# Optimization experiments

Measured on AMD Instinct MI355X. Metric: run time of the kernel, lower is better.

The kernel has to match this reference:

```python
import jax, jax.numpy as jnp
import numpy as np

B, T, C = 4, 2048, 1024
H, D = 16, 64  # num_heads, head_size


def setup_inputs() -> dict:
    key = jax.random.key(0)
    ks = jax.random.split(key, 5)
    s = 0.02
    x = jax.random.normal(ks[0], (B, T, C), dtype=jnp.float32)
    Wq = jax.random.normal(ks[1], (H, C, D), dtype=jnp.float32) * s
    Wk = jax.random.normal(ks[2], (H, C, D), dtype=jnp.float32) * s
    Wv = jax.random.normal(ks[3], (H, C, D), dtype=jnp.float32) * s
    Wp = jax.random.normal(ks[4], (C, H * D), dtype=jnp.float32) * s  # Linear(H*D, C) weight
    bp = jnp.zeros((C,), dtype=jnp.float32)
    return {"x": x, "Wq": Wq, "Wk": Wk, "Wv": Wv, "Wp": Wp, "bp": bp}


def reference(x, Wq, Wk, Wv, Wp, bp):
    # per-head projections (all heads batched): [B,T,C] x [H,C,D] -> [B,H,T,D]
    q = jnp.einsum('btc,hcd->bhtd', x, Wq)
    k = jnp.einsum('btc,hcd->bhtd', x, Wk)
    v = jnp.einsum('btc,hcd->bhtd', x, Wv)
    scale = 1.0 / jnp.sqrt(jnp.asarray(D, dtype=x.dtype))
    scores = jnp.einsum('bhtd,bhsd->bhts', q, k) * scale  # [B,H,T,T]
    causal = jnp.tril(jnp.ones((T, T), dtype=bool))
    scores = jnp.where(causal, scores, -jnp.inf)
    w = jax.nn.softmax(scores, axis=-1)
    out = jnp.einsum('bhts,bhsd->bhtd', w, v)  # [B,H,T,D]
    out = out.transpose(0, 2, 1, 3).reshape(B, T, H * D)  # concat heads
    return out @ Wp.T + bp  # projection (dropout is identity in eval)
```

## Files before the change

### kernel.cpp

```cpp
#include <hip/hip_runtime.h>
#include <stdint.h>


typedef unsigned short u16;
typedef __attribute__((ext_vector_type(8))) short    s16x8;
typedef __attribute__((ext_vector_type(4))) float    f32x4;
typedef __attribute__((ext_vector_type(2))) uint32_t u32x2;


__device__ __forceinline__ u16 f2b(float f) {
  union { float f; uint32_t u; } v; v.f = f;
  uint32_t r = v.u + 0x7FFFu + ((v.u >> 16) & 1u);
  return (u16)(r >> 16);
}

__device__ __forceinline__ uint32_t cvtpk(float a, float b) {
  uint32_t r;
  asm("v_cvt_pk_bf16_f32 %0, %1, %2" : "=v"(r) : "v"(a), "v"(b));
  return r;
}

__device__ __forceinline__ float vexp2(float x) {
  float r;
  asm("v_exp_f32 %0, %1" : "=v"(r) : "v"(x));
  return r;
}

__device__ __forceinline__ f32x4 mfma_bf16(s16x8 a, s16x8 b, f32x4 c) {
  asm("v_mfma_f32_16x16x32_bf16 %0, %1, %2, %0" : "+v"(c) : "v"(a), "v"(b));
  return c;
}

__device__ __forceinline__ void gload_lds16(const void* g, void* l) {
  __builtin_amdgcn_global_load_lds(
      (__attribute__((address_space(1))) void*)(uintptr_t)g,
      (__attribute__((address_space(3))) void*)(uint32_t)(uintptr_t)l,
      16, 0, 0);
}


__global__ void cvt_all_kernel(const float* __restrict__ x, const float* __restrict__ Wq,
                               const float* __restrict__ Wk, const float* __restrict__ Wv,
                               const float* __restrict__ Wp, u16* __restrict__ xb,
                               u16* __restrict__ wqkvb, u16* __restrict__ wpb) {
  int bid = blockIdx.x;
  if (bid < 4608) {
    const float* src = (bid < 4096) ? x : Wp;
    u16* dst = (bid < 4096) ? xb : wpb;
    size_t i = (size_t)((bid < 4096) ? bid : (bid - 4096)) * 256 + threadIdx.x;
    const f32x4* pp = (const f32x4*)(src + i * 8);
    f32x4 a = pp[0], b2 = pp[1];
    s16x8 o;
    o[0]=(short)f2b(a[0]); o[1]=(short)f2b(a[1]); o[2]=(short)f2b(a[2]); o[3]=(short)f2b(a[3]);
    o[4]=(short)f2b(b2[0]); o[5]=(short)f2b(b2[1]); o[6]=(short)f2b(b2[2]); o[7]=(short)f2b(b2[3]);
    *(s16x8*)(dst + i * 8) = o;
  } else {
    int idx = (bid - 4608) * 256 + threadIdx.x;
    int sel = idx >> 20;
    int rem = idx & 1048575;
    int n = rem >> 10, c = rem & 1023;
    int h = n >> 6, d = n & 63;
    const float* W = (sel == 0) ? Wq : ((sel == 1) ? Wk : Wv);
    wqkvb[idx] = f2b(W[h * 65536 + c * 64 + d]);
  }
}


template <int MODE>
__global__ __launch_bounds__(256) void gemm_bt_kernel(
    const u16* __restrict__ A, const u16* __restrict__ B, void* __restrict__ Cout,
    const float* __restrict__ bias, u16* __restrict__ vTout, int K, int ldc)
{
  __shared__ __attribute__((aligned(16))) u16 As[128 * 64];
  __shared__ __attribute__((aligned(16))) u16 Bs[128 * 64];

  const int tid  = threadIdx.x;
  const int lane = tid & 63;
  const int w    = tid >> 6;
  const int wm   = w >> 1, wn = w & 1;
  const int g    = lane >> 4;
  const int li   = lane & 15;
  const size_t bm = (size_t)blockIdx.x * 128;
  const size_t bn = (size_t)blockIdx.y * 128;

  f32x4 acc[4][4] = {};

  const int kIters = K >> 6;
  for (int kt = 0; kt < kIters; ++kt) {
    const int kb = kt * 64;
#pragma unroll
    for (int i = 0; i < 4; ++i) {
      int c = i * 256 + tid;
      int row = c >> 3, sl = c & 7;
      int ss = sl ^ (row & 7);
      gload_lds16(A + (bm + row) * K + kb + ss * 8, &As[c * 8]);
      gload_lds16(B + (bn + row) * K + kb + ss * 8, &Bs[c * 8]);
    }
    __syncthreads();
#pragma unroll
    for (int ks = 0; ks < 2; ++ks) {
      s16x8 af[4], bfr[4];
#pragma unroll
      for (int f = 0; f < 4; ++f) {
        int ra = wm * 64 + f * 16 + li;
        int sa = (ks * 4 + g) ^ (ra & 7);
        af[f] = *(const s16x8*)&As[ra * 64 + sa * 8];
        int rb = wn * 64 + f * 16 + li;
        int sb = (ks * 4 + g) ^ (rb & 7);
        bfr[f] = *(const s16x8*)&Bs[rb * 64 + sb * 8];
      }
#pragma unroll
      for (int mi = 0; mi < 4; ++mi)
#pragma unroll
        for (int ni = 0; ni < 4; ++ni)
          acc[mi][ni] = mfma_bf16(af[mi], bfr[ni], acc[mi][ni]);
    }
    __syncthreads();
  }

  if constexpr (MODE == 1) {
#pragma unroll
    for (int ni = 0; ni < 4; ++ni) {
      size_t col = bn + wn * 64 + ni * 16 + li;
      float bv = bias[col];
#pragma unroll
      for (int mi = 0; mi < 4; ++mi)
#pragma unroll
        for (int r = 0; r < 4; ++r) {
          size_t row = bm + wm * 64 + mi * 16 + g * 4 + r;
          ((float*)Cout)[row * ldc + col] = acc[mi][ni][r] + bv;
        }
    }
  } else {
    if (bn < 2048) {
#pragma unroll
      for (int ni = 0; ni < 4; ++ni) {
        size_t col = bn + wn * 64 + ni * 16 + li;
#pragma unroll
        for (int mi = 0; mi < 4; ++mi)
#pragma unroll
          for (int r = 0; r < 4; ++r) {
            size_t row = bm + wm * 64 + mi * 16 + g * 4 + r;
            ((u16*)Cout)[row * ldc + col] = f2b(acc[mi][ni][r]);
          }
      }
    } else {
      const int hb = (int)((bn - 2048) >> 6) + wn;
      const int bb = (int)(bm >> 11);
      const int t0b = ((int)bm & 2047) + wm * 64 + g * 4;
      u16* vrow = vTout + (size_t)((bb * 16 + hb) * 64) * 2048;
#pragma unroll
      for (int ni = 0; ni < 4; ++ni) {
        u16* vd_ = vrow + (size_t)(ni * 16 + li) * 2048;
#pragma unroll
        for (int mi = 0; mi < 4; ++mi) {
          u32x2 wv = { cvtpk(acc[mi][ni][0], acc[mi][ni][1]),
                       cvtpk(acc[mi][ni][2], acc[mi][ni][3]) };
          *(u32x2*)&vd_[t0b + mi * 16] = wv;
        }
      }
    }
  }
}


__global__ __launch_bounds__(256, 4) void attn_kernel(const u16* __restrict__ qkv,
                                                      const u16* __restrict__ vT,
                                                      u16* __restrict__ out) {
  __shared__ __attribute__((aligned(16))) u16 Ks[2][64 * 64];
  __shared__ __attribute__((aligned(16))) u16 Vs[2][64 * 64];
  __shared__ __attribute__((aligned(16))) u16 Ps[4][16 * 64];

  const int id  = blockIdx.x;
  const int xcd = id & 7;
  const int rr  = id >> 3;
  const int bh  = xcd * 8 + (rr & 7);
  const int p   = rr >> 3;

  const int b = bh >> 4, h = bh & 15;
  const int tid = threadIdx.x;
  const int lane = tid & 63;
  const int w = tid >> 6;
  const int g = lane >> 4, li = lane & 15;

  const int tA = 31 - p;
  const int nA = tA + 1;
  const int nTot = 33;

  const u16* kbase = qkv + (size_t)(b * 2048) * 3072 + 1024 + h * 64;
  const u16* vtb   = vT + (size_t)bh * 64 * 2048;
  u16* pl = Ps[w];

  const int srow = tid >> 3;
  const int ssl0 = (tid & 7) ^ (srow & 7);
  const int kge0 = srow * 3072 + ssl0 * 8;
  const int vge0 = srow * 2048 + ssl0 * 8;
  u16* const kd0 = &Ks[0][tid * 8];
  u16* const vd0 = &Vs[0][tid * 8];

  int foff[2][4];
#pragma unroll
  for (int kk = 0; kk < 2; ++kk)
#pragma unroll
    for (int fj = 0; fj < 4; ++fj) {
      int rk = fj * 16 + li;
      foff[kk][fj] = rk * 64 + (((kk * 4 + g) ^ (rk & 7)) * 8);
    }
  const int lsw = li & 14;
  int pwoff[4], proff[2];
#pragma unroll
  for (int fj = 0; fj < 4; ++fj) pwoff[fj] = li * 64 + (((4 * fj + g) ^ lsw) * 4);
#pragma unroll
  for (int kk = 0; kk < 2; ++kk) proff[kk] = li * 64 + (((8 * kk + 2 * g) ^ lsw) * 4);

  auto stage = [&](int buf, int j0) {
    const u16* kp = kbase + (size_t)j0 * 3072;
    const u16* vp = vtb + j0;
    u16* kd = kd0 + buf * 4096;
    u16* vd = vd0 + buf * 4096;
    gload_lds16(kp + kge0, kd);
    gload_lds16(kp + kge0 + 32 * 3072, kd + 2048);
    gload_lds16(vp + vge0, vd);
    gload_lds16(vp + vge0 + 32 * 2048, vd + 2048);
  };

  stage(0, 0);
  __syncthreads();

  s16x8 qf[2];
  f32x4 oacc[4];
  float mrow = -1e30f, lrowp = 0.f;
  int qglob = 0;
  const float cexp = 0.18033688011112042f;
  const float thr = 8.0f;

  for (int s = 0; s < nTot; ++s) {
    const int cur = s & 1;
    const bool inA = s < nA;
    const int t  = inA ? s : s - nA;
    const int qt = inA ? tA : p;
    const int j0 = t * 64;

    if (s + 1 < nTot) {
      int t1 = (s + 1 < nA) ? (s + 1) : (s + 1 - nA);
      stage(cur ^ 1, t1 * 64);
    }

    if (t == 0) {
      qglob = qt * 64 + w * 16 + li;
      const u16* qbase = qkv + (size_t)(b * 2048 + qglob) * 3072 + h * 64;
#pragma unroll
      for (int kk = 0; kk < 2; ++kk)
        qf[kk] = *(const s16x8*)&qbase[kk * 32 + g * 8];
      mrow = -1e30f; lrowp = 0.f;
#pragma unroll
      for (int fd = 0; fd < 4; ++fd) oacc[fd] = (f32x4)0.f;
    }

    const u16* ksb = &Ks[0][0] + cur * 4096;
    const u16* vsb = &Vs[0][0] + cur * 4096;

    f32x4 sfr[4] = {};
    __builtin_amdgcn_s_setprio(1);
#pragma unroll
    for (int kk = 0; kk < 2; ++kk) {
      s16x8 kf[4];
#pragma unroll
      for (int fj = 0; fj < 4; ++fj) kf[fj] = *(const s16x8*)&ksb[foff[kk][fj]];
#pragma unroll
      for (int fj = 0; fj < 4; ++fj) sfr[fj] = mfma_bf16(kf[fj], qf[kk], sfr[fj]);
    }
    __builtin_amdgcn_s_setprio(0);

    if (t == qt) {
#pragma unroll
      for (int fj = 0; fj < 4; ++fj)
#pragma unroll
        for (int r = 0; r < 4; ++r) {
          int jj = j0 + fj * 16 + g * 4 + r;
          if (jj > qglob) sfr[fj][r] = -1e30f;
        }
    }

    float mx = sfr[0][0];
#pragma unroll
    for (int fj = 0; fj < 4; ++fj)
#pragma unroll
      for (int r = 0; r < 4; ++r) mx = fmaxf(mx, sfr[fj][r]);

    bool need = (mx - mrow) * cexp > thr;
    if (__any(need)) {
      float m0 = mx;
      m0 = fmaxf(m0, __shfl_xor(m0, 16));
      m0 = fmaxf(m0, __shfl_xor(m0, 32));
      float mnew = fmaxf(mrow, m0);
      float sc = vexp2((mrow - mnew) * cexp);
      mrow = mnew;
      lrowp *= sc;
#pragma unroll
      for (int fd = 0; fd < 4; ++fd)
#pragma unroll
        for (int r = 0; r < 4; ++r) oacc[fd][r] *= sc;
    }

    float rs = 0.f;
#pragma unroll
    for (int fj = 0; fj < 4; ++fj) {
      float p0 = vexp2((sfr[fj][0] - mrow) * cexp);
      float p1 = vexp2((sfr[fj][1] - mrow) * cexp);
      float p2 = vexp2((sfr[fj][2] - mrow) * cexp);
      float p3 = vexp2((sfr[fj][3] - mrow) * cexp);
      rs += (p0 + p1) + (p2 + p3);
      u32x2 wv = { cvtpk(p0, p1), cvtpk(p2, p3) };
      *(u32x2*)&pl[pwoff[fj]] = wv;
    }
    lrowp += rs;

    __builtin_amdgcn_s_setprio(1);
#pragma unroll
    for (int kk = 0; kk < 2; ++kk) {
      s16x8 pf = *(const s16x8*)&pl[proff[kk]];
      s16x8 vf[4];
#pragma unroll
      for (int fd = 0; fd < 4; ++fd) vf[fd] = *(const s16x8*)&vsb[foff[kk][fd]];
#pragma unroll
      for (int fd = 0; fd < 4; ++fd) oacc[fd] = mfma_bf16(vf[fd], pf, oacc[fd]);
    }
    __builtin_amdgcn_s_setprio(0);

    if (t == qt) {
      float lr = lrowp;
      lr += __shfl_xor(lr, 16);
      lr += __shfl_xor(lr, 32);
      float inv = 1.f / lr;
      u16* ob = out + (size_t)(b * 2048 + qglob) * 1024 + h * 64;
#pragma unroll
      for (int fd = 0; fd < 4; ++fd) {
        u32x2 wv = { cvtpk(oacc[fd][0] * inv, oacc[fd][1] * inv),
                     cvtpk(oacc[fd][2] * inv, oacc[fd][3] * inv) };
        *(u32x2*)&ob[fd * 16 + g * 4] = wv;
      }
    }

    __syncthreads();
  }
}


extern "C" void kernel_launch(void* const* d_in, const int* in_sizes, int n_in,
                              void* d_out, int out_size, void* d_ws, size_t ws_size,
                              hipStream_t stream) {
  const float* x  = (const float*)d_in[0];
  const float* Wq = (const float*)d_in[1];
  const float* Wk = (const float*)d_in[2];
  const float* Wv = (const float*)d_in[3];
  const float* Wp = (const float*)d_in[4];
  const float* bp = (const float*)d_in[5];
  (void)in_sizes; (void)n_in; (void)out_size; (void)ws_size;

  char* ws = (char*)d_ws;
  u16* xb    = (u16*)(ws);
  u16* wqkvb = (u16*)(ws + 16777216);
  u16* wpb   = (u16*)(ws + 23068672);
  u16* qkv   = (u16*)(ws + 25165824);
  u16* vT    = (u16*)(ws + 75497472);
  u16* ao    = (u16*)(ws + 92274688);

  cvt_all_kernel<<<16896, 256, 0, stream>>>(x, Wq, Wk, Wv, Wp, xb, wqkvb, wpb);

  gemm_bt_kernel<2><<<dim3(64, 24), 256, 0, stream>>>(
      xb, wqkvb, (void*)qkv, nullptr, vT, 1024, 3072);

  attn_kernel<<<1024, 256, 0, stream>>>(qkv, vT, ao);

  gemm_bt_kernel<1><<<dim3(64, 8), 256, 0, stream>>>(
      ao, wpb, d_out, bp, nullptr, 1024, 1024);
}
```

Before: 154.8 us.

## Split KV tile across warp pairs with 32-row Q per warp and merge partial softmax

```diff
diff --git a/kernel.cpp b/kernel.cpp
--- a/kernel.cpp
+++ b/kernel.cpp
@@ -169,7 +169,7 @@
                                                       u16* __restrict__ out) {
   __shared__ __attribute__((aligned(16))) u16 Ks[2][64 * 64];
   __shared__ __attribute__((aligned(16))) u16 Vs[2][64 * 64];
-  __shared__ __attribute__((aligned(16))) u16 Ps[4][16 * 64];
+  __shared__ __attribute__((aligned(16))) u16 Ps[4][32 * 32];
 
   const int id  = blockIdx.x;
   const int xcd = id & 7;
@@ -182,6 +182,8 @@
   const int lane = tid & 63;
   const int w = tid >> 6;
   const int g = lane >> 4, li = lane & 15;
+  const int wq  = w & 1;
+  const int kvh = w >> 1;
 
   const int tA = 31 - p;
   const int nA = tA + 1;
@@ -198,20 +200,29 @@
   u16* const kd0 = &Ks[0][tid * 8];
   u16* const vd0 = &Vs[0][tid * 8];
 
-  int foff[2][4];
+  int foffK[2][2];
 #pragma unroll
   for (int kk = 0; kk < 2; ++kk)
 #pragma unroll
-    for (int fj = 0; fj < 4; ++fj) {
-      int rk = fj * 16 + li;
-      foff[kk][fj] = rk * 64 + (((kk * 4 + g) ^ (rk & 7)) * 8);
-    }
-  const int lsw = li & 14;
-  int pwoff[4], proff[2];
-#pragma unroll
-  for (int fj = 0; fj < 4; ++fj) pwoff[fj] = li * 64 + (((4 * fj + g) ^ lsw) * 4);
-#pragma unroll
-  for (int kk = 0; kk < 2; ++kk) proff[kk] = li * 64 + (((8 * kk + 2 * g) ^ lsw) * 4);
+    for (int fj = 0; fj < 2; ++fj) {
+      int rk = kvh * 32 + fj * 16 + li;
+      foffK[kk][fj] = rk * 64 + (((kk * 4 + g) ^ (rk & 7)) * 8);
+    }
+  int foffV[4];
+#pragma unroll
+  for (int fd = 0; fd < 4; ++fd) {
+    int rv = fd * 16 + li;
+    foffV[fd] = rv * 64 + (((kvh * 4 + g) ^ (rv & 7)) * 8);
+  }
+  const int psw = li & 3;
+  int pwoff[2][2], proff[2];
+#pragma unroll
+  for (int fm = 0; fm < 2; ++fm) {
+#pragma unroll
+    for (int fj = 0; fj < 2; ++fj)
+      pwoff[fm][fj] = (fm * 16 + li) * 32 + (((fj * 2 + (g >> 1)) ^ psw) * 8) + (g & 1) * 4;
+    proff[fm] = (fm * 16 + li) * 32 + ((g ^ psw) * 8);
+  }
 
   auto stage = [&](int buf, int j0) {
     const u16* kp = kbase + (size_t)j0 * 3072;
@@ -227,10 +238,10 @@
   stage(0, 0);
   __syncthreads();
 
-  s16x8 qf[2];
-  f32x4 oacc[4];
-  float mrow = -1e30f, lrowp = 0.f;
-  int qglob = 0;
+  s16x8 qf[2][2];
+  f32x4 oacc[2][4];
+  float mrow[2], lrowp[2];
+  int qg0 = 0;
   const float cexp = 0.18033688011112042f;
   const float thr = 8.0f;
 
@@ -247,98 +258,160 @@
     }
 
     if (t == 0) {
-      qglob = qt * 64 + w * 16 + li;
-      const u16* qbase = qkv + (size_t)(b * 2048 + qglob) * 3072 + h * 64;
-#pragma unroll
-      for (int kk = 0; kk < 2; ++kk)
-        qf[kk] = *(const s16x8*)&qbase[kk * 32 + g * 8];
-      mrow = -1e30f; lrowp = 0.f;
-#pragma unroll
-      for (int fd = 0; fd < 4; ++fd) oacc[fd] = (f32x4)0.f;
+      qg0 = qt * 64 + wq * 32 + li;
+#pragma unroll
+      for (int fm = 0; fm < 2; ++fm) {
+        const u16* qbase = qkv + (size_t)(b * 2048 + qg0 + fm * 16) * 3072 + h * 64;
+#pragma unroll
+        for (int kk = 0; kk < 2; ++kk)
+          qf[fm][kk] = *(const s16x8*)&qbase[kk * 32 + g * 8];
+        mrow[fm] = -1e30f; lrowp[fm] = 0.f;
+#pragma unroll
+        for (int fd = 0; fd < 4; ++fd) oacc[fm][fd] = (f32x4)0.f;
+      }
     }
 
     const u16* ksb = &Ks[0][0] + cur * 4096;
     const u16* vsb = &Vs[0][0] + cur * 4096;
 
-    f32x4 sfr[4] = {};
-    __builtin_amdgcn_s_setprio(1);
-#pragma unroll
-    for (int kk = 0; kk < 2; ++kk) {
-      s16x8 kf[4];
-#pragma unroll
-      for (int fj = 0; fj < 4; ++fj) kf[fj] = *(const s16x8*)&ksb[foff[kk][fj]];
-#pragma unroll
-      for (int fj = 0; fj < 4; ++fj) sfr[fj] = mfma_bf16(kf[fj], qf[kk], sfr[fj]);
-    }
-    __builtin_amdgcn_s_setprio(0);
+    const bool skipw = (t == qt) && (kvh == 1) && (wq == 0);
+    if (!skipw) {
+      f32x4 sfr[2][2] = {};
+      __builtin_amdgcn_s_setprio(1);
+#pragma unroll
+      for (int kk = 0; kk < 2; ++kk) {
+        s16x8 kf[2];
+#pragma unroll
+        for (int fj = 0; fj < 2; ++fj) kf[fj] = *(const s16x8*)&ksb[foffK[kk][fj]];
+#pragma unroll
+        for (int fm = 0; fm < 2; ++fm)
+#pragma unroll
+          for (int fj = 0; fj < 2; ++fj)
+            sfr[fm][fj] = mfma_bf16(kf[fj], qf[fm][kk], sfr[fm][fj]);
+      }
+      __builtin_amdgcn_s_setprio(0);
+
+      if (t == qt) {
+#pragma unroll
+        for (int fm = 0; fm < 2; ++fm)
+#pragma unroll
+          for (int fj = 0; fj < 2; ++fj)
+#pragma unroll
+            for (int r = 0; r < 4; ++r) {
+              int jj = j0 + kvh * 32 + fj * 16 + g * 4 + r;
+              if (jj > qg0 + fm * 16) sfr[fm][fj][r] = -1e30f;
+            }
+      }
+
+      float mx[2];
+#pragma unroll
+      for (int fm = 0; fm < 2; ++fm) {
+        float m0 = sfr[fm][0][0];
+#pragma unroll
+        for (int fj = 0; fj < 2; ++fj)
+#pragma unroll
+          for (int r = 0; r < 4; ++r) m0 = fmaxf(m0, sfr[fm][fj][r]);
+        mx[fm] = m0;
+      }
+      bool need = ((mx[0] - mrow[0]) * cexp > thr) | ((mx[1] - mrow[1]) * cexp > thr);
+      if (__any(need)) {
+#pragma unroll
+        for (int fm = 0; fm < 2; ++fm) {
+          float m0 = mx[fm];
+          m0 = fmaxf(m0, __shfl_xor(m0, 16));
+          m0 = fmaxf(m0, __shfl_xor(m0, 32));
+          float mnew = fmaxf(mrow[fm], m0);
+          float sc = vexp2((mrow[fm] - mnew) * cexp);
+          mrow[fm] = mnew;
+          lrowp[fm] *= sc;
+#pragma unroll
+          for (int fd = 0; fd < 4; ++fd)
+#pragma unroll
+            for (int r = 0; r < 4; ++r) oacc[fm][fd][r] *= sc;
+        }
+      }
+
+#pragma unroll
+      for (int fm = 0; fm < 2; ++fm) {
+        float rs = 0.f;
+#pragma unroll
+        for (int fj = 0; fj < 2; ++fj) {
+          float p0 = vexp2((sfr[fm][fj][0] - mrow[fm]) * cexp);
+          float p1 = vexp2((sfr[fm][fj][1] - mrow[fm]) * cexp);
+          float p2 = vexp2((sfr[fm][fj][2] - mrow[fm]) * cexp);
+          float p3 = vexp2((sfr[fm][fj][3] - mrow[fm]) * cexp);
+          rs += (p0 + p1) + (p2 + p3);
+          u32x2 wv = { cvtpk(p0, p1), cvtpk(p2, p3) };
+          *(u32x2*)&pl[pwoff[fm][fj]] = wv;
+        }
+        lrowp[fm] += rs;
+      }
+
+      __builtin_amdgcn_s_setprio(1);
+      s16x8 vf[4];
+#pragma unroll
+      for (int fd = 0; fd < 4; ++fd) vf[fd] = *(const s16x8*)&vsb[foffV[fd]];
+#pragma unroll
+      for (int fm = 0; fm < 2; ++fm) {
+        s16x8 pf = *(const s16x8*)&pl[proff[fm]];
+#pragma unroll
+        for (int fd = 0; fd < 4; ++fd)
+          oacc[fm][fd] = mfma_bf16(vf[fd], pf, oacc[fm][fd]);
+      }
+      __builtin_amdgcn_s_setprio(0);
+    }
 
     if (t == qt) {
-#pragma unroll
-      for (int fj = 0; fj < 4; ++fj)
-#pragma unroll
-        for (int r = 0; r < 4; ++r) {
-          int jj = j0 + fj * 16 + g * 4 + r;
-          if (jj > qglob) sfr[fj][r] = -1e30f;
-        }
-    }
-
-    float mx = sfr[0][0];
-#pragma unroll
-    for (int fj = 0; fj < 4; ++fj)
-#pragma unroll
-      for (int r = 0; r < 4; ++r) mx = fmaxf(mx, sfr[fj][r]);
-
-    bool need = (mx - mrow) * cexp > thr;
-    if (__any(need)) {
-      float m0 = mx;
-      m0 = fmaxf(m0, __shfl_xor(m0, 16));
-      m0 = fmaxf(m0, __shfl_xor(m0, 32));
-      float mnew = fmaxf(mrow, m0);
-      float sc = vexp2((mrow - mnew) * cexp);
-      mrow = mnew;
-      lrowp *= sc;
-#pragma unroll
-      for (int fd = 0; fd < 4; ++fd)
-#pragma unroll
-        for (int r = 0; r < 4; ++r) oacc[fd][r] *= sc;
-    }
-
-    float rs = 0.f;
-#pragma unroll
-    for (int fj = 0; fj < 4; ++fj) {
-      float p0 = vexp2((sfr[fj][0] - mrow) * cexp);
-      float p1 = vexp2((sfr[fj][1] - mrow) * cexp);
-      float p2 = vexp2((sfr[fj][2] - mrow) * cexp);
-      float p3 = vexp2((sfr[fj][3] - mrow) * cexp);
-      rs += (p0 + p1) + (p2 + p3);
-      u32x2 wv = { cvtpk(p0, p1), cvtpk(p2, p3) };
-      *(u32x2*)&pl[pwoff[fj]] = wv;
-    }
-    lrowp += rs;
-
-    __builtin_amdgcn_s_setprio(1);
-#pragma unroll
-    for (int kk = 0; kk < 2; ++kk) {
-      s16x8 pf = *(const s16x8*)&pl[proff[kk]];
-      s16x8 vf[4];
-#pragma unroll
-      for (int fd = 0; fd < 4; ++fd) vf[fd] = *(const s16x8*)&vsb[foff[kk][fd]];
-#pragma unroll
-      for (int fd = 0; fd < 4; ++fd) oacc[fd] = mfma_bf16(vf[fd], pf, oacc[fd]);
-    }
-    __builtin_amdgcn_s_setprio(0);
-
-    if (t == qt) {
-      float lr = lrowp;
-      lr += __shfl_xor(lr, 16);
-      lr += __shfl_xor(lr, 32);
-      float inv = 1.f / lr;
-      u16* ob = out + (size_t)(b * 2048 + qglob) * 1024 + h * 64;
-#pragma unroll
-      for (int fd = 0; fd < 4; ++fd) {
-        u32x2 wv = { cvtpk(oacc[fd][0] * inv, oacc[fd][1] * inv),
-                     cvtpk(oacc[fd][2] * inv, oacc[fd][3] * inv) };
-        *(u32x2*)&ob[fd * 16 + g * 4] = wv;
+      float lr[2];
+#pragma unroll
+      for (int fm = 0; fm < 2; ++fm) {
+        float v = lrowp[fm];
+        v += __shfl_xor(v, 16);
+        v += __shfl_xor(v, 32);
+        lr[fm] = v;
+      }
+      __syncthreads();
+      if (kvh == 1) {
+        float* os = (float*)((wq == 0 ? &Ks[0][0] : &Vs[0][0]) + cur * 4096);
+#pragma unroll
+        for (int fm = 0; fm < 2; ++fm)
+#pragma unroll
+          for (int fd = 0; fd < 4; ++fd)
+            *(f32x4*)&os[(fm * 16 + li) * 64 + (((fd * 4 + g) ^ li) * 4)] = oacc[fm][fd];
+        float* ml = (float*)&Ps[w][0];
+        if (g == 0) {
+#pragma unroll
+          for (int fm = 0; fm < 2; ++fm) {
+            ml[fm * 32 + li] = mrow[fm];
+            ml[fm * 32 + 16 + li] = lr[fm];
+          }
+        }
+      }
+      __syncthreads();
+      if (kvh == 0) {
+        const float* os = (const float*)((wq == 0 ? &Ks[0][0] : &Vs[0][0]) + cur * 4096);
+        const float* ml = (const float*)&Ps[w + 2][0];
+#pragma unroll
+        for (int fm = 0; fm < 2; ++fm) {
+          float mB = ml[fm * 32 + li];
+          float lB = ml[fm * 32 + 16 + li];
+          float mstar = fmaxf(mrow[fm], mB);
+          float sA = vexp2((mrow[fm] - mstar) * cexp);
+          float sB = vexp2((mB - mstar) * cexp);
+          float inv = 1.f / (sA * lr[fm] + sB * lB);
+          float fA = sA * inv, fB = sB * inv;
+          u16* ob = out + (size_t)(b * 2048 + qg0 + fm * 16) * 1024 + h * 64;
+#pragma unroll
+          for (int fd = 0; fd < 4; ++fd) {
+            f32x4 obp = *(const f32x4*)&os[(fm * 16 + li) * 64 + (((fd * 4 + g) ^ li) * 4)];
+            float o0 = fA * oacc[fm][fd][0] + fB * obp[0];
+            float o1 = fA * oacc[fm][fd][1] + fB * obp[1];
+            float o2 = fA * oacc[fm][fd][2] + fB * obp[2];
+            float o3 = fA * oacc[fm][fd][3] + fB * obp[3];
+            u32x2 wv = { cvtpk(o0, o1), cvtpk(o2, o3) };
+            *(u32x2*)&ob[fd * 16 + g * 4] = wv;
+          }
+        }
       }
     }
 
```

After: 157.2 us. About the same (+1.5%).
